# Kernel tuning notes

Hardware: AMD Instinct MI355X
Metric: run time of the kernel (lower is better)

Reference implementation:

```python
import jax, jax.numpy as jnp
import numpy as np

G = 9.80665  # scipy.constants.g


def _xavier(key, fan_in, fan_out):
    std = np.sqrt(2.0 / (fan_in + fan_out))
    return jax.random.normal(key, (fan_in, fan_out), dtype=jnp.float32) * std


def setup_inputs() -> dict:
    key = jax.random.key(0)
    ks = jax.random.split(key, 16)
    n_samples, n_nodes, n_pipes, n_demand, hidden = 16384, 512, 1024, 256, 64
    D = jax.random.uniform(ks[0], (n_samples, n_demand), dtype=jnp.float32) * 0.01
    leak_id = jax.random.randint(ks[1], (n_samples, 1), 0, n_pipes)
    A0 = jax.random.normal(ks[2], (n_nodes, n_pipes), dtype=jnp.float32) * 0.1
    inv = jax.random.normal(ks[3], (n_nodes, n_pipes), dtype=jnp.float32) * 0.1
    M = jax.random.normal(ks[4], (n_nodes, n_pipes), dtype=jnp.float32) * 0.1
    supply = jax.random.uniform(ks[5], (n_pipes,), dtype=jnp.float32) * 10.0
    L = jax.random.uniform(ks[6], (n_pipes,), dtype=jnp.float32) * 900.0 + 100.0  # pipe length [m]
    d = jax.random.uniform(ks[7], (n_pipes,), dtype=jnp.float32) * 0.4 + 0.1      # diameter [m]
    C = jax.random.uniform(ks[8], (n_pipes,), dtype=jnp.float32) * 50.0 + 100.0   # HW coefficient
    demand_idx = jnp.arange(n_demand) * 2  # distinct node indices < n_nodes
    a = jnp.float32(0.01)   # leak area
    Cd = jnp.float32(0.75)  # discharge coefficient
    W1 = _xavier(ks[9], 1, hidden); b1 = jnp.zeros((hidden,), jnp.float32)
    W2 = _xavier(ks[10], hidden, hidden); b2 = jnp.zeros((hidden,), jnp.float32)
    W3 = _xavier(ks[11], hidden, 1); b3 = jnp.zeros((1,), jnp.float32)
    base = jax.random.normal(ks[12], (n_pipes,), dtype=jnp.float32) * 0.1
    return {"D": D, "leak_id": leak_id, "A0": A0, "inv": inv, "M": M,
            "supply": supply, "L": L, "d": d, "C": C, "a": a, "Cd": Cd,
            "W1": W1, "b1": b1, "W2": W2, "b2": b2, "W3": W3, "b3": b3,
            "base": base, "demand_idx": demand_idx}


def reference(D, leak_id, A0, inv, M, supply, L, d, C, a, Cd,
              W1, b1, W2, b2, W3, b3, base, demand_idx):
    S = D.shape[0]
    n_nodes, n_pipes = M.shape
    idx = leak_id[:, 0]  # [S] int, pipe index per sample

    # Net(leak_id): tanh MLP + lookup of per-pipe base value
    x = leak_id.astype(jnp.float32)                      # [S,1]
    h = jnp.tanh(x @ W1 + b1)
    h = jnp.tanh(h @ W2 + b2)
    net_out = base[idx][:, None] + (h @ W3 + b3)          # [S,1]

    # scatter-built demand / leakage / areas
    demand = jnp.zeros((S, n_nodes), jnp.float32).at[:, demand_idx].set(D)
    rows = jnp.arange(S)
    leakage = jnp.zeros((S, n_pipes), jnp.float32).at[rows, idx].set(net_out[:, 0])
    areas = jnp.zeros((S, n_pipes), jnp.float32).at[rows, idx].set(a)

    # q = inv.T @ (M @ leakage + demand)
    y = jnp.einsum('np,sp->sn', M, leakage) + demand      # [S,Nn]
    q = jnp.einsum('np,sn->sp', inv, y)                   # [S,Np]

    # Hazen-Williams head loss
    hL = jnp.sign(q) * 10.667 * C[None] ** (-1.852) * d[None] ** (-4.871) * L[None] * jnp.abs(q) ** 1.852
    H = jnp.einsum('np,sp->sn', inv, supply[None] - hL)   # [S,Nn]

    # leak demand d_leak = Cd * (M @ areas) * sqrt(2 g relu(H))  (safe sqrt)
    Hp = jax.nn.relu(H)
    sq = jnp.sqrt(jnp.where(Hp > 0, Hp, 1.0)) * (Hp > 0).astype(jnp.float32)
    d_leak = Cd * jnp.einsum('np,sp->sn', M, areas) * jnp.sqrt(jnp.float32(2.0 * G)) * sq

    residual = jnp.einsum('np,sp->sn', A0, q) - demand - d_leak
    return jnp.mean(residual ** 2)
```

## Files before the change

kernel.cpp:

```cpp
#include <hip/hip_runtime.h>
#include <math.h>

typedef _Float16 f16;
typedef _Float16 f16x4 __attribute__((ext_vector_type(4)));
typedef _Float16 f16x8 __attribute__((ext_vector_type(8)));
typedef float f32x4 __attribute__((ext_vector_type(4)));

#define S_TOTAL 16384
#define N_NODES 512
#define N_PIPES 1024
#define N_DEM   256
#define HIDDEN  64
#define T_SCALE 256.0f

#define GLOAD16(gsrc, ldst) \
    __builtin_amdgcn_global_load_lds((const __attribute__((address_space(1))) void*)(gsrc), \
                                     (__attribute__((address_space(3))) void*)(ldst), 16, 0, 0)
#define SBAR()  __builtin_amdgcn_s_barrier()
#define FENCE() asm volatile("" ::: "memory")
#define WAIT4() asm volatile("s_waitcnt vmcnt(4)" ::: "memory")
#define WAIT0() asm volatile("s_waitcnt vmcnt(0)" ::: "memory")

__global__ __launch_bounds__(256) void prep_all(
    const float* __restrict__ W1, const float* __restrict__ b1,
    const float* __restrict__ W2, const float* __restrict__ b2,
    const float* __restrict__ W3, const float* __restrict__ b3,
    const float* __restrict__ base,
    const float* __restrict__ L, const float* __restrict__ dpipe,
    const float* __restrict__ Cw,
    const float* __restrict__ Mf, const float* __restrict__ inv,
    const float* __restrict__ A0, const float* __restrict__ D,
    const int* __restrict__ dmap,
    float* __restrict__ net, float* __restrict__ lKc,
    f16* __restrict__ MT16, f16* __restrict__ invT16,
    f16* __restrict__ inv16, f16* __restrict__ A016, f16* __restrict__ D16,
    f16* __restrict__ DI16, f16* __restrict__ IDXT,
    float* __restrict__ out, int out_size)
{
    __shared__ __align__(16) f16 tile[64][72];
    const int b = blockIdx.x, t = threadIdx.x;
    if (b < 256) {
        if (b == 0) for (int i = t; i < out_size; i += 256) out[i] = 0.f;
        const int wid = t >> 6, k = t & 63;
        const int p = b * 4 + wid;
        const float x = (float)p;
        float h1 = tanhf(x * W1[k] + b1[k]);
        float acc = b2[k];
        #pragma unroll
        for (int j = 0; j < HIDDEN; ++j) {
            float hj = __shfl(h1, j, 64);
            acc = fmaf(hj, W2[j * HIDDEN + k], acc);
        }
        float partial = tanhf(acc) * W3[k];
        #pragma unroll
        for (int off = 32; off > 0; off >>= 1) partial += __shfl_down(partial, off, 64);
        if (k == 0) {
            net[p] = base[p] + partial + b3[0];
            lKc[p] = log2f(10.667f) - 1.852f * log2f(Cw[p]) - 4.871f * log2f(dpipe[p]) + log2f(L[p]);
        }
        return;
    }
    if (b < 512) {
        const int idx = b - 256;
        const float* in = (idx < 128) ? Mf : inv;
        f16* outp = (idx < 128) ? MT16 : invT16;
        const int i2 = idx & 127;
        const int bx = i2 & 15, by = i2 >> 4;
        const int r0 = by * 64, c0 = bx * 64;
        const int lr = t / 16, lc4 = (t % 16) * 4;
        #pragma unroll
        for (int i = 0; i < 4; ++i) {
            int r = lr + i * 16;
            float4 v = *(const float4*)(in + (size_t)(r0 + r) * N_PIPES + c0 + lc4);
            tile[lc4 + 0][r] = (f16)v.x; tile[lc4 + 1][r] = (f16)v.y;
            tile[lc4 + 2][r] = (f16)v.z; tile[lc4 + 3][r] = (f16)v.w;
        }
        __syncthreads();
        const int wrow = t / 4, wc16 = (t % 4) * 16;
        *(f16x8*)(outp + (size_t)(c0 + wrow) * N_NODES + r0 + wc16)     = *(f16x8*)&tile[wrow][wc16];
        *(f16x8*)(outp + (size_t)(c0 + wrow) * N_NODES + r0 + wc16 + 8) = *(f16x8*)&tile[wrow][wc16 + 8];
        return;
    }
    const int tid = (b - 512) * 256 + t;
    const int np = 768 * 256;
    for (int i = tid; i < (N_NODES * N_PIPES) / 4; i += np) {
        float4 v = ((const float4*)inv)[i];
        ((f16x4*)inv16)[i] = (f16x4){(f16)v.x, (f16)v.y, (f16)v.z, (f16)v.w};
        float4 w = ((const float4*)A0)[i];
        ((f16x4*)A016)[i] = (f16x4){(f16)w.x, (f16)w.y, (f16)w.z, (f16)w.w};
    }
    for (int i = tid; i < (S_TOTAL * N_DEM) / 4; i += np) {
        float4 v = ((const float4*)D)[i];
        ((f16x4*)D16)[i] = (f16x4){(f16)v.x, (f16)v.y, (f16)v.z, (f16)v.w};
    }
    for (int i = tid; i < N_DEM * (N_PIPES / 4); i += np) {
        int j = i >> 8, p0 = (i & 255) * 4;
        float4 v = *(const float4*)(inv + (size_t)dmap[j] * N_PIPES + p0);
        *(f16x4*)(DI16 + (size_t)j * N_PIPES + p0) = (f16x4){(f16)v.x, (f16)v.y, (f16)v.z, (f16)v.w};
    }
    for (int i = tid; i < N_PIPES * (N_DEM / 4); i += np) {
        int p = i >> 6, j0 = (i & 63) * 4;
        f16x4 o;
        #pragma unroll
        for (int u = 0; u < 4; ++u)
            o[u] = (f16)inv[(size_t)dmap[j0 + u] * N_PIPES + p];
        *(f16x4*)(IDXT + (size_t)p * N_DEM + j0) = o;
    }
}

struct GemmP {
    const f16* A; int lda;
    const f16* B; int ldb;
    f16* C; int ldc;
    int K;
    const int* dmap;
    int gx, gy;
};

__device__ __forceinline__ void gemm_body(const GemmP& P, int bx, int by) {
    __shared__ __align__(16) f16 As[128][72], Bs[64][72];
    const int m0 = by * 128, c0 = bx * 64;
    const int t = threadIdx.x, lane = t & 63, wid = t >> 6;
    const int wr = wid >> 1, wc = wid & 1;
    const int cl = lane & 15, g = lane >> 4;
    const int tr = t >> 3, tc = (t & 7) * 8;
    f32x4 acc[4][2] = {};
    for (int k0 = 0; k0 < P.K; k0 += 64) {
        #pragma unroll
        for (int r = 0; r < 4; ++r) {
            int row = r * 32 + tr;
            *(f16x8*)&As[row][tc] = *(const f16x8*)(P.A + (size_t)(m0 + row) * P.lda + k0 + tc);
        }
        #pragma unroll
        for (int r = 0; r < 2; ++r) {
            int row = r * 32 + tr;
            *(f16x8*)&Bs[row][tc] = *(const f16x8*)(P.B + (size_t)(c0 + row) * P.ldb + k0 + tc);
        }
        __syncthreads();
        #pragma unroll
        for (int kk = 0; kk < 2; ++kk) {
            const int kb = kk * 32 + g * 8;
            f16x8 a[4], bfr[2];
            #pragma unroll
            for (int m = 0; m < 4; ++m) a[m] = *(const f16x8*)&As[wr * 64 + m * 16 + cl][kb];
            #pragma unroll
            for (int n = 0; n < 2; ++n) bfr[n] = *(const f16x8*)&Bs[wc * 32 + n * 16 + cl][kb];
            #pragma unroll
            for (int m = 0; m < 4; ++m)
                #pragma unroll
                for (int n = 0; n < 2; ++n)
                    acc[m][n] = __builtin_amdgcn_mfma_f32_16x16x32_f16(a[m], bfr[n], acc[m][n], 0, 0, 0);
        }
        __syncthreads();
    }
    #pragma unroll
    for (int m = 0; m < 4; ++m)
        #pragma unroll
        for (int reg = 0; reg < 4; ++reg) {
            const int row = m0 + wr * 64 + m * 16 + g * 4 + reg;
            #pragma unroll
            for (int n = 0; n < 2; ++n) {
                const int col = c0 + wc * 32 + n * 16 + cl;
                float v = acc[m][n][reg];
                if (P.dmap && P.dmap[col] == row) v -= 1.0f;
                P.C[(size_t)row * P.ldc + col] = (f16)v;
            }
        }
}

__global__ __launch_bounds__(256) void gemm_small3(GemmP p0, GemmP p1, GemmP p2) {
    const GemmP& P = (blockIdx.z == 0) ? p0 : (blockIdx.z == 1) ? p1 : p2;
    if ((int)blockIdx.x >= P.gx || (int)blockIdx.y >= P.gy) return;
    gemm_body(P, blockIdx.x, blockIdx.y);
}

__global__ __launch_bounds__(256) void gemm_small1(GemmP p0) {
    gemm_body(p0, blockIdx.x, blockIdx.y);
}

__global__ __launch_bounds__(512, 4) void gemm_qt_mfma(
    const f16* __restrict__ D16, const int* __restrict__ leak_id,
    const f16* __restrict__ IDXT, const float* __restrict__ net,
    const f16* __restrict__ G16, const float* __restrict__ lKc,
    const float* __restrict__ supply, f16* __restrict__ t16)
{
    __shared__ __align__(16) f16 As[2][128][64];
    __shared__ __align__(16) f16 Bs[2][128][64];
    const int nwg = gridDim.x * gridDim.y;
    const int bid = blockIdx.y * gridDim.x + blockIdx.x;
    const int w = (bid & 7) * (nwg >> 3) + (bid >> 3);
    const int bx = w % gridDim.x, by = w / gridDim.x;
    const int p0 = bx * 128, sb = by * 128;
    const int t = threadIdx.x, lane = t & 63, wid = t >> 6;
    const int wr = wid >> 2, wc = wid & 3;
    const int cl = lane & 15, g = lane >> 4;
    const int swrow = lane >> 3;
    const int swcol = ((lane & 7) ^ swrow) * 8;
    const int sx0 = ((g) ^ (cl & 7)) * 8;
    const int sx1 = ((4 + g) ^ (cl & 7)) * 8;

    const f16* Abase = D16 + (size_t)(sb + swrow) * N_DEM + swcol;
    const f16* Bbase = IDXT + (size_t)(p0 + swrow) * N_DEM + swcol;

    f32x4 acc[4][2] = {};
    auto stage = [&](int buf, int k0) {
        #pragma unroll
        for (int c = 0; c < 2; ++c) {
            int r0 = c * 64 + wid * 8;
            GLOAD16(Abase + (size_t)r0 * N_DEM + k0, &As[buf][r0][0]);
        }
        #pragma unroll
        for (int c = 0; c < 2; ++c) {
            int r0 = c * 64 + wid * 8;
            GLOAD16(Bbase + (size_t)r0 * N_DEM + k0, &Bs[buf][r0][0]);
        }
    };
    auto compute = [&](int buf) {
        #pragma unroll
        for (int kk = 0; kk < 2; ++kk) {
            const int sx = kk ? sx1 : sx0;
            f16x8 a[4], b[2];
            #pragma unroll
            for (int m = 0; m < 4; ++m) a[m] = *(const f16x8*)&As[buf][wr * 64 + m * 16 + cl][sx];
            #pragma unroll
            for (int n = 0; n < 2; ++n) b[n] = *(const f16x8*)&Bs[buf][wc * 32 + n * 16 + cl][sx];
            #pragma unroll
            for (int m = 0; m < 4; ++m)
                #pragma unroll
                for (int n = 0; n < 2; ++n)
                    acc[m][n] = __builtin_amdgcn_mfma_f32_16x16x32_f16(a[m], b[n], acc[m][n], 0, 0, 0);
        }
    };

    int cur = 0;
    stage(0, 0);
    #pragma unroll 1
    for (int k = 0; k < 3; ++k) {
        stage(cur ^ 1, (k + 1) * 64);
        WAIT4(); SBAR();
        compute(cur);
        FENCE(); SBAR();
        cur ^= 1;
    }
    WAIT0(); SBAR();
    compute(cur);

    float lKc2[2], sup2[2]; int pcol[2];
    #pragma unroll
    for (int n = 0; n < 2; ++n) {
        pcol[n] = p0 + wc * 32 + n * 16 + cl;
        lKc2[n] = lKc[pcol[n]]; sup2[n] = supply[pcol[n]];
    }
    #pragma unroll
    for (int m = 0; m < 4; ++m) {
        #pragma unroll
        for (int reg = 0; reg < 4; ++reg) {
            const int srow = sb + wr * 64 + m * 16 + g * 4 + reg;
            const int idx = leak_id[srow];
            const float nv = net[idx];
            #pragma unroll
            for (int n = 0; n < 2; ++n) {
                float qv = acc[m][n][reg] + nv * (float)G16[(size_t)idx * N_PIPES + pcol[n]];
                float l = __builtin_amdgcn_logf(fabsf(qv));
                float hL = copysignf(__builtin_amdgcn_exp2f(fmaf(1.852f, l, lKc2[n])), qv);
                t16[(size_t)srow * N_PIPES + pcol[n]] = (f16)((sup2[n] - hL) * (1.0f / T_SCALE));
            }
        }
    }
}

__global__ __launch_bounds__(512, 4) void gemm_res_mfma(
    const f16* __restrict__ t16, const f16* __restrict__ inv16,
    const f16* __restrict__ D16, const f16* __restrict__ P1p,
    const f16* __restrict__ MT16, const f16* __restrict__ G2_16,
    const int* __restrict__ leak_id, const float* __restrict__ net,
    const float* __restrict__ Cd_p, const float* __restrict__ a_p,
    float scale, float* __restrict__ out)
{
    __shared__ __align__(16) f16 As[2][128][64];
    __shared__ __align__(16) f16 Bs[2][128][64];
    const int nwg = gridDim.x * gridDim.y;
    const int bid = blockIdx.y * gridDim.x + blockIdx.x;
    const int w = (bid & 7) * (nwg >> 3) + (bid >> 3);
    const int bx = w % gridDim.x, by = w / gridDim.x;
    const int n0 = bx * 128, sb = by * 128;
    const int t = threadIdx.x, lane = t & 63, wid = t >> 6;
    const int wr = wid >> 2, wc = wid & 3;
    const int cl = lane & 15, g = lane >> 4;
    const int swrow = lane >> 3;
    const int swcol = ((lane & 7) ^ swrow) * 8;
    const int sx0 = ((g) ^ (cl & 7)) * 8;
    const int sx1 = ((4 + g) ^ (cl & 7)) * 8;

    const f16* HAb = t16   + (size_t)(sb + swrow) * N_PIPES + swcol;
    const f16* HBb = inv16 + (size_t)(n0 + swrow) * N_PIPES + swcol;
    const f16* RAb = D16   + (size_t)(sb + swrow) * N_DEM + swcol;
    const f16* RBb = P1p   + (size_t)(n0 + swrow) * N_DEM + swcol;

    f32x4 accH[4][2] = {}, accR[4][2] = {};

    auto stageH = [&](int buf, int k0) {
        #pragma unroll
        for (int c = 0; c < 2; ++c) {
            int r0 = c * 64 + wid * 8;
            GLOAD16(HAb + (size_t)r0 * N_PIPES + k0, &As[buf][r0][0]);
        }
        #pragma unroll
        for (int c = 0; c < 2; ++c) {
            int r0 = c * 64 + wid * 8;
            GLOAD16(HBb + (size_t)r0 * N_PIPES + k0, &Bs[buf][r0][0]);
        }
    };
    auto stageR = [&](int buf, int k0) {
        #pragma unroll
        for (int c = 0; c < 2; ++c) {
            int r0 = c * 64 + wid * 8;
            GLOAD16(RAb + (size_t)r0 * N_DEM + k0, &As[buf][r0][0]);
        }
        #pragma unroll
        for (int c = 0; c < 2; ++c) {
            int r0 = c * 64 + wid * 8;
            GLOAD16(RBb + (size_t)r0 * N_DEM + k0, &Bs[buf][r0][0]);
        }
    };
    auto computeT = [&](int buf, f32x4 (&accA)[4][2]) {
        #pragma unroll
        for (int kk = 0; kk < 2; ++kk) {
            const int sx = kk ? sx1 : sx0;
            f16x8 a[4], b[2];
            #pragma unroll
            for (int m = 0; m < 4; ++m) a[m] = *(const f16x8*)&As[buf][wr * 64 + m * 16 + cl][sx];
            #pragma unroll
            for (int n = 0; n < 2; ++n) b[n] = *(const f16x8*)&Bs[buf][wc * 32 + n * 16 + cl][sx];
            #pragma unroll
            for (int m = 0; m < 4; ++m)
                #pragma unroll
                for (int n = 0; n < 2; ++n)
                    accA[m][n] = __builtin_amdgcn_mfma_f32_16x16x32_f16(a[m], b[n], accA[m][n], 0, 0, 0);
        }
    };

    int cur = 0;
    stageH(0, 0);
    #pragma unroll 1
    for (int k = 0; k < 15; ++k) {
        stageH(cur ^ 1, (k + 1) * 64);
        WAIT4(); SBAR();
        computeT(cur, accH);
        FENCE(); SBAR();
        cur ^= 1;
    }
    stageR(cur ^ 1, 0);
    WAIT4(); SBAR();
    computeT(cur, accH);
    FENCE(); SBAR();
    cur ^= 1;
    #pragma unroll 1
    for (int k = 0; k < 3; ++k) {
        stageR(cur ^ 1, (k + 1) * 64);
        WAIT4(); SBAR();
        computeT(cur, accR);
        FENCE(); SBAR();
        cur ^= 1;
    }
    WAIT0(); SBAR();
    computeT(cur, accR);

    const float cda = Cd_p[0] * a_p[0] * sqrtf(2.f * 9.80665f);
    int node[2];
    #pragma unroll
    for (int n = 0; n < 2; ++n) node[n] = n0 + wc * 32 + n * 16 + cl;
    float lsum = 0.f;
    #pragma unroll
    for (int m = 0; m < 4; ++m) {
        #pragma unroll
        for (int reg = 0; reg < 4; ++reg) {
            const int srow = sb + wr * 64 + m * 16 + g * 4 + reg;
            const int idx = leak_id[srow];
            const float nv = net[idx];
            #pragma unroll
            for (int n = 0; n < 2; ++n) {
                const float H = accH[m][n][reg] * T_SCALE;
                const float sq = (H > 0.f) ? sqrtf(H) : 0.f;
                const float dl = cda * (float)MT16[(size_t)idx * N_NODES + node[n]] * sq;
                const float r = accR[m][n][reg] + nv * (float)G2_16[(size_t)idx * N_NODES + node[n]] - dl;
                lsum += r * r;
            }
        }
    }
    #pragma unroll
    for (int off = 32; off > 0; off >>= 1) lsum += __shfl_down(lsum, off, 64);
    __syncthreads();
    float* wred = (float*)&As[0][0][0];
    if (lane == 0) wred[wid] = lsum;
    __syncthreads();
    if (t == 0) {
        float tot = 0.f;
        #pragma unroll
        for (int i = 0; i < 8; ++i) tot += wred[i];
        atomicAdd(out, tot * scale);
    }
}

extern "C" void kernel_launch(void* const* d_in, const int* in_sizes, int n_in,
                              void* d_out, int out_size, void* d_ws, size_t ws_size,
                              hipStream_t stream) {
    const float* D          = (const float*)d_in[0];
    const int*   leak_id    = (const int*)  d_in[1];
    const float* A0         = (const float*)d_in[2];
    const float* inv        = (const float*)d_in[3];
    const float* M          = (const float*)d_in[4];
    const float* supply     = (const float*)d_in[5];
    const float* L          = (const float*)d_in[6];
    const float* dpipe      = (const float*)d_in[7];
    const float* C          = (const float*)d_in[8];
    const float* a_p        = (const float*)d_in[9];
    const float* Cd_p       = (const float*)d_in[10];
    const float* W1         = (const float*)d_in[11];
    const float* b1         = (const float*)d_in[12];
    const float* W2         = (const float*)d_in[13];
    const float* b2         = (const float*)d_in[14];
    const float* W3         = (const float*)d_in[15];
    const float* b3         = (const float*)d_in[16];
    const float* base       = (const float*)d_in[17];
    const int*   demand_idx = (const int*)  d_in[18];

    char* ws = (char*)d_ws;
    size_t off = 0;
    auto carve = [&](size_t bytes) { char* p = ws + off; off += (bytes + 255) & ~(size_t)255; return p; };
    float* net    = (float*)carve(N_PIPES * 4);
    float* lKc    = (float*)carve(N_PIPES * 4);
    f16* inv16  = (f16*)carve((size_t)N_NODES * N_PIPES * 2);
    f16* A016   = (f16*)carve((size_t)N_NODES * N_PIPES * 2);
    f16* MT16   = (f16*)carve((size_t)N_PIPES * N_NODES * 2);
    f16* invT16 = (f16*)carve((size_t)N_PIPES * N_NODES * 2);
    f16* G16    = (f16*)carve((size_t)N_PIPES * N_PIPES * 2);
    f16* G2_16  = (f16*)carve((size_t)N_PIPES * N_NODES * 2);
    f16* Wt     = (f16*)carve((size_t)N_NODES * N_NODES * 2);
    f16* P1p    = (f16*)carve((size_t)N_NODES * N_DEM * 2);
    f16* DI16   = (f16*)carve((size_t)N_DEM * N_PIPES * 2);
    f16* IDXT   = (f16*)carve((size_t)N_PIPES * N_DEM * 2);
    f16* D16    = (f16*)carve((size_t)S_TOTAL * N_DEM * 2);
    f16* t16    = (f16*)carve((size_t)S_TOTAL * N_PIPES * 2);

    prep_all<<<1280, 256, 0, stream>>>(
        W1, b1, W2, b2, W3, b3, base, L, dpipe, C,
        M, inv, A0, D, demand_idx,
        net, lKc, MT16, invT16, inv16, A016, D16, DI16, IDXT,
        (float*)d_out, out_size);

    GemmP pG16 = {MT16, N_NODES, invT16, N_NODES, G16, N_PIPES, N_NODES, nullptr, 16, 8};
    GemmP pWt  = {A016, N_PIPES, inv16, N_PIPES, Wt, N_NODES, N_PIPES, nullptr, 8, 4};
    GemmP pP1  = {A016, N_PIPES, DI16, N_PIPES, P1p, N_DEM, N_PIPES, demand_idx, 4, 4};
    gemm_small3<<<dim3(16, 8, 3), 256, 0, stream>>>(pG16, pWt, pP1);

    GemmP pG2 = {MT16, N_NODES, Wt, N_NODES, G2_16, N_NODES, N_NODES, nullptr, 8, 8};
    gemm_small1<<<dim3(8, 8), 256, 0, stream>>>(pG2);

    gemm_qt_mfma<<<dim3(N_PIPES / 128, S_TOTAL / 128), 512, 0, stream>>>(
        D16, leak_id, IDXT, net, G16, lKc, supply, t16);
    const float scale = 1.f / ((float)S_TOTAL * (float)N_NODES);
    gemm_res_mfma<<<dim3(N_NODES / 128, S_TOTAL / 128), 512, 0, stream>>>(
        t16, inv16, D16, P1p, MT16, G2_16, leak_id, net, Cd_p, a_p,
        scale, (float*)d_out);
}
```

Measured before the change: 97.16 us.

## Convert D to fp16 inside GEMM tiles and fold G2 GEMM into qt launch

The separate fp16 conversion of D in the prep kernel is removed. The q-GEMM and the residual GEMM now load fp32 D rows from global memory, convert them in registers and write them into a single swizzled LDS tile, using a new wait/barrier pipeline. The small MT·Wt GEMM (G2) is no longer its own launch; it runs as extra blocks appended to the q-GEMM grid (blockIdx.y >= 128). This saves one launch, the D16 write/read round trip and some prep work, but it reads twice as many bytes for D and adds register-staged loads with manual vmcnt accounting, which risks ordering mistakes.

```diff
diff --git a/kernel.cpp b/kernel.cpp
--- a/kernel.cpp
+++ b/kernel.cpp
@@ -18,8 +18,8 @@
                                      (__attribute__((address_space(3))) void*)(ldst), 16, 0, 0)
 #define SBAR()  __builtin_amdgcn_s_barrier()
 #define FENCE() asm volatile("" ::: "memory")
-#define WAIT4() asm volatile("s_waitcnt vmcnt(4)" ::: "memory")
-#define WAIT0() asm volatile("s_waitcnt vmcnt(0)" ::: "memory")
+#define WAITN(n) asm volatile("s_waitcnt vmcnt(" #n ")" ::: "memory")
+#define LGKM0() asm volatile("s_waitcnt lgkmcnt(0)" ::: "memory")
 
 __global__ __launch_bounds__(256) void prep_all(
     const float* __restrict__ W1, const float* __restrict__ b1,
@@ -29,11 +29,11 @@
     const float* __restrict__ L, const float* __restrict__ dpipe,
     const float* __restrict__ Cw,
     const float* __restrict__ Mf, const float* __restrict__ inv,
-    const float* __restrict__ A0, const float* __restrict__ D,
+    const float* __restrict__ A0,
     const int* __restrict__ dmap,
     float* __restrict__ net, float* __restrict__ lKc,
     f16* __restrict__ MT16, f16* __restrict__ invT16,
-    f16* __restrict__ inv16, f16* __restrict__ A016, f16* __restrict__ D16,
+    f16* __restrict__ inv16, f16* __restrict__ A016,
     f16* __restrict__ DI16, f16* __restrict__ IDXT,
     float* __restrict__ out, int out_size)
 {
@@ -82,16 +82,12 @@
         return;
     }
     const int tid = (b - 512) * 256 + t;
-    const int np = 768 * 256;
+    const int np = 512 * 256;
     for (int i = tid; i < (N_NODES * N_PIPES) / 4; i += np) {
         float4 v = ((const float4*)inv)[i];
         ((f16x4*)inv16)[i] = (f16x4){(f16)v.x, (f16)v.y, (f16)v.z, (f16)v.w};
         float4 w = ((const float4*)A0)[i];
         ((f16x4*)A016)[i] = (f16x4){(f16)w.x, (f16)w.y, (f16)w.z, (f16)w.w};
-    }
-    for (int i = tid; i < (S_TOTAL * N_DEM) / 4; i += np) {
-        float4 v = ((const float4*)D)[i];
-        ((f16x4*)D16)[i] = (f16x4){(f16)v.x, (f16)v.y, (f16)v.z, (f16)v.w};
     }
     for (int i = tid; i < N_DEM * (N_PIPES / 4); i += np) {
         int j = i >> 8, p0 = (i & 255) * 4;
@@ -174,56 +170,103 @@
     gemm_body(P, blockIdx.x, blockIdx.y);
 }
 
-__global__ __launch_bounds__(256) void gemm_small1(GemmP p0) {
-    gemm_body(p0, blockIdx.x, blockIdx.y);
-}
-
 __global__ __launch_bounds__(512, 4) void gemm_qt_mfma(
-    const f16* __restrict__ D16, const int* __restrict__ leak_id,
+    const float* __restrict__ Df, const int* __restrict__ leak_id,
     const f16* __restrict__ IDXT, const float* __restrict__ net,
     const f16* __restrict__ G16, const float* __restrict__ lKc,
-    const float* __restrict__ supply, f16* __restrict__ t16)
+    const float* __restrict__ supply, f16* __restrict__ t16,
+    const f16* __restrict__ MT16, const f16* __restrict__ Wt,
+    f16* __restrict__ G2out)
 {
-    __shared__ __align__(16) f16 As[2][128][64];
-    __shared__ __align__(16) f16 Bs[2][128][64];
-    const int nwg = gridDim.x * gridDim.y;
-    const int bid = blockIdx.y * gridDim.x + blockIdx.x;
-    const int w = (bid & 7) * (nwg >> 3) + (bid >> 3);
-    const int bx = w % gridDim.x, by = w / gridDim.x;
+    __shared__ __align__(16) f16 AsM[128 * 64];
+    __shared__ __align__(16) f16 BsM[2][128 * 64];
+    const int t = threadIdx.x, lane = t & 63, wid = t >> 6;
+
+    if (blockIdx.y >= 128) {
+        f16 (*A2)[72] = (f16(*)[72])&BsM[0][0];
+        f16 (*B2)[72] = (f16(*)[72])&AsM[0];
+        const int m0 = ((int)blockIdx.y - 128) * 128, c0 = blockIdx.x * 64;
+        const int wr = wid >> 2, wc = wid & 3;
+        const int cl = lane & 15, g = lane >> 4;
+        f32x4 acc[4] = {};
+        for (int k0 = 0; k0 < 512; k0 += 64) {
+            {
+                int r = t >> 2, c16 = (t & 3) * 16;
+                *(f16x8*)&A2[r][c16]     = *(const f16x8*)(MT16 + (size_t)(m0 + r) * N_NODES + k0 + c16);
+                *(f16x8*)&A2[r][c16 + 8] = *(const f16x8*)(MT16 + (size_t)(m0 + r) * N_NODES + k0 + c16 + 8);
+                int r2 = t >> 3, c8 = (t & 7) * 8;
+                *(f16x8*)&B2[r2][c8] = *(const f16x8*)(Wt + (size_t)(c0 + r2) * N_NODES + k0 + c8);
+            }
+            __syncthreads();
+            #pragma unroll
+            for (int kk = 0; kk < 2; ++kk) {
+                const int kb = kk * 32 + g * 8;
+                f16x8 b = *(const f16x8*)&B2[wc * 16 + cl][kb];
+                #pragma unroll
+                for (int m = 0; m < 4; ++m) {
+                    f16x8 a = *(const f16x8*)&A2[wr * 64 + m * 16 + cl][kb];
+                    acc[m] = __builtin_amdgcn_mfma_f32_16x16x32_f16(a, b, acc[m], 0, 0, 0);
+                }
+            }
+            __syncthreads();
+        }
+        #pragma unroll
+        for (int m = 0; m < 4; ++m)
+            #pragma unroll
+            for (int reg = 0; reg < 4; ++reg)
+                G2out[(size_t)(m0 + wr * 64 + m * 16 + g * 4 + reg) * N_NODES + c0 + wc * 16 + cl] = (f16)acc[m][reg];
+        return;
+    }
+    const int bid = blockIdx.y * 8 + blockIdx.x;
+    const int w = (bid & 7) * 128 + (bid >> 3);
+    const int bx = w & 7, by = w >> 3;
     const int p0 = bx * 128, sb = by * 128;
-    const int t = threadIdx.x, lane = t & 63, wid = t >> 6;
     const int wr = wid >> 2, wc = wid & 3;
     const int cl = lane & 15, g = lane >> 4;
     const int swrow = lane >> 3;
-    const int swcol = ((lane & 7) ^ swrow) * 8;
-    const int sx0 = ((g) ^ (cl & 7)) * 8;
-    const int sx1 = ((4 + g) ^ (cl & 7)) * 8;
-
-    const f16* Abase = D16 + (size_t)(sb + swrow) * N_DEM + swcol;
-    const f16* Bbase = IDXT + (size_t)(p0 + swrow) * N_DEM + swcol;
-
-    f32x4 acc[4][2] = {};
-    auto stage = [&](int buf, int k0) {
+    const int swp = ((lane & 7) ^ swrow) * 8;
+    const int sx0 = (g ^ (cl & 7)) * 8, sx1 = ((4 + g) ^ (cl & 7)) * 8;
+
+    f16 (*As)[64] = (f16(*)[64])AsM;
+    const f16* Bbase = IDXT + (size_t)(p0 + swrow) * N_DEM + swp;
+
+    const int arow = t >> 2, ah = t & 3;
+    const int s0 = 2 * ah, s1 = 2 * ah + 1;
+    const int gc0 = (s0 ^ (arow & 7)) * 8, gc1 = (s1 ^ (arow & 7)) * 8;
+    const float* Drow = Df + (size_t)(sb + arow) * N_DEM;
+
+    float4 a01, a02, a11, a12;
+    auto A_load = [&](int k0) {
+        a01 = *(const float4*)(Drow + k0 + gc0);
+        a02 = *(const float4*)(Drow + k0 + gc0 + 4);
+        a11 = *(const float4*)(Drow + k0 + gc1);
+        a12 = *(const float4*)(Drow + k0 + gc1 + 4);
+    };
+    auto A_write = [&]() {
+        f16x8 v0 = {(f16)a01.x, (f16)a01.y, (f16)a01.z, (f16)a01.w,
+                    (f16)a02.x, (f16)a02.y, (f16)a02.z, (f16)a02.w};
+        f16x8 v1 = {(f16)a11.x, (f16)a11.y, (f16)a11.z, (f16)a11.w,
+                    (f16)a12.x, (f16)a12.y, (f16)a12.z, (f16)a12.w};
+        *(f16x8*)&As[arow][s0 * 8] = v0;
+        *(f16x8*)&As[arow][s1 * 8] = v1;
+    };
+    auto B_stage = [&](int buf, int k0) {
         #pragma unroll
         for (int c = 0; c < 2; ++c) {
             int r0 = c * 64 + wid * 8;
-            GLOAD16(Abase + (size_t)r0 * N_DEM + k0, &As[buf][r0][0]);
-        }
-        #pragma unroll
-        for (int c = 0; c < 2; ++c) {
-            int r0 = c * 64 + wid * 8;
-            GLOAD16(Bbase + (size_t)r0 * N_DEM + k0, &Bs[buf][r0][0]);
-        }
-    };
+            GLOAD16(Bbase + (size_t)r0 * N_DEM + k0, &BsM[buf][r0 * 64]);
+        }
+    };
+    f32x4 acc[4][2] = {};
     auto compute = [&](int buf) {
         #pragma unroll
         for (int kk = 0; kk < 2; ++kk) {
             const int sx = kk ? sx1 : sx0;
             f16x8 a[4], b[2];
             #pragma unroll
-            for (int m = 0; m < 4; ++m) a[m] = *(const f16x8*)&As[buf][wr * 64 + m * 16 + cl][sx];
-            #pragma unroll
-            for (int n = 0; n < 2; ++n) b[n] = *(const f16x8*)&Bs[buf][wc * 32 + n * 16 + cl][sx];
+            for (int m = 0; m < 4; ++m) a[m] = *(const f16x8*)&As[wr * 64 + m * 16 + cl][sx];
+            #pragma unroll
+            for (int n = 0; n < 2; ++n) b[n] = *(const f16x8*)&BsM[buf][(wc * 32 + n * 16 + cl) * 64 + sx];
             #pragma unroll
             for (int m = 0; m < 4; ++m)
                 #pragma unroll
@@ -232,18 +275,19 @@
         }
     };
 
+    A_load(0); B_stage(0, 0);
     int cur = 0;
-    stage(0, 0);
     #pragma unroll 1
-    for (int k = 0; k < 3; ++k) {
-        stage(cur ^ 1, (k + 1) * 64);
-        WAIT4(); SBAR();
+    for (int k = 0; k < 4; ++k) {
+        WAITN(2);
+        SBAR();
+        A_write(); LGKM0();
+        if (k < 3) { A_load((k + 1) * 64); B_stage(cur ^ 1, (k + 1) * 64); WAITN(6); }
+        else       { WAITN(0); }
+        SBAR();
         compute(cur);
-        FENCE(); SBAR();
         cur ^= 1;
     }
-    WAIT0(); SBAR();
-    compute(cur);
 
     float lKc2[2], sup2[2]; int pcol[2];
     #pragma unroll
@@ -271,14 +315,14 @@
 
 __global__ __launch_bounds__(512, 4) void gemm_res_mfma(
     const f16* __restrict__ t16, const f16* __restrict__ inv16,
-    const f16* __restrict__ D16, const f16* __restrict__ P1p,
+    const float* __restrict__ Df, const f16* __restrict__ P1p,
     const f16* __restrict__ MT16, const f16* __restrict__ G2_16,
     const int* __restrict__ leak_id, const float* __restrict__ net,
     const float* __restrict__ Cd_p, const float* __restrict__ a_p,
     float scale, float* __restrict__ out)
 {
-    __shared__ __align__(16) f16 As[2][128][64];
-    __shared__ __align__(16) f16 Bs[2][128][64];
+    __shared__ __align__(16) f16 AsM[2][128 * 64];
+    __shared__ __align__(16) f16 BsM[2][128 * 64];
     const int nwg = gridDim.x * gridDim.y;
     const int bid = blockIdx.y * gridDim.x + blockIdx.x;
     const int w = (bid & 7) * (nwg >> 3) + (bid >> 3);
@@ -288,14 +332,12 @@
     const int wr = wid >> 2, wc = wid & 3;
     const int cl = lane & 15, g = lane >> 4;
     const int swrow = lane >> 3;
-    const int swcol = ((lane & 7) ^ swrow) * 8;
-    const int sx0 = ((g) ^ (cl & 7)) * 8;
-    const int sx1 = ((4 + g) ^ (cl & 7)) * 8;
-
-    const f16* HAb = t16   + (size_t)(sb + swrow) * N_PIPES + swcol;
-    const f16* HBb = inv16 + (size_t)(n0 + swrow) * N_PIPES + swcol;
-    const f16* RAb = D16   + (size_t)(sb + swrow) * N_DEM + swcol;
-    const f16* RBb = P1p   + (size_t)(n0 + swrow) * N_DEM + swcol;
+    const int swp = ((lane & 7) ^ swrow) * 8;
+    const int sx0 = (g ^ (cl & 7)) * 8, sx1 = ((4 + g) ^ (cl & 7)) * 8;
+
+    const f16* HAb = t16   + (size_t)(sb + swrow) * N_PIPES + swp;
+    const f16* HBb = inv16 + (size_t)(n0 + swrow) * N_PIPES + swp;
+    const f16* RBb = P1p   + (size_t)(n0 + swrow) * N_DEM + swp;
 
     f32x4 accH[4][2] = {}, accR[4][2] = {};
 
@@ -303,40 +345,28 @@
         #pragma unroll
         for (int c = 0; c < 2; ++c) {
             int r0 = c * 64 + wid * 8;
-            GLOAD16(HAb + (size_t)r0 * N_PIPES + k0, &As[buf][r0][0]);
+            GLOAD16(HAb + (size_t)r0 * N_PIPES + k0, &AsM[buf][r0 * 64]);
         }
         #pragma unroll
         for (int c = 0; c < 2; ++c) {
             int r0 = c * 64 + wid * 8;
-            GLOAD16(HBb + (size_t)r0 * N_PIPES + k0, &Bs[buf][r0][0]);
-        }
-    };
-    auto stageR = [&](int buf, int k0) {
-        #pragma unroll
-        for (int c = 0; c < 2; ++c) {
-            int r0 = c * 64 + wid * 8;
-            GLOAD16(RAb + (size_t)r0 * N_DEM + k0, &As[buf][r0][0]);
-        }
-        #pragma unroll
-        for (int c = 0; c < 2; ++c) {
-            int r0 = c * 64 + wid * 8;
-            GLOAD16(RBb + (size_t)r0 * N_DEM + k0, &Bs[buf][r0][0]);
-        }
-    };
-    auto computeT = [&](int buf, f32x4 (&accA)[4][2]) {
+            GLOAD16(HBb + (size_t)r0 * N_PIPES + k0, &BsM[buf][r0 * 64]);
+        }
+    };
+    auto computeH = [&](int buf) {
         #pragma unroll
         for (int kk = 0; kk < 2; ++kk) {
             const int sx = kk ? sx1 : sx0;
             f16x8 a[4], b[2];
             #pragma unroll
-            for (int m = 0; m < 4; ++m) a[m] = *(const f16x8*)&As[buf][wr * 64 + m * 16 + cl][sx];
-            #pragma unroll
-            for (int n = 0; n < 2; ++n) b[n] = *(const f16x8*)&Bs[buf][wc * 32 + n * 16 + cl][sx];
+            for (int m = 0; m < 4; ++m) a[m] = *(const f16x8*)&AsM[buf][(wr * 64 + m * 16 + cl) * 64 + sx];
+            #pragma unroll
+            for (int n = 0; n < 2; ++n) b[n] = *(const f16x8*)&BsM[buf][(wc * 32 + n * 16 + cl) * 64 + sx];
             #pragma unroll
             for (int m = 0; m < 4; ++m)
                 #pragma unroll
                 for (int n = 0; n < 2; ++n)
-                    accA[m][n] = __builtin_amdgcn_mfma_f32_16x16x32_f16(a[m], b[n], accA[m][n], 0, 0, 0);
+                    accH[m][n] = __builtin_amdgcn_mfma_f32_16x16x32_f16(a[m], b[n], accH[m][n], 0, 0, 0);
         }
     };
 
@@ -345,26 +375,73 @@
     #pragma unroll 1
     for (int k = 0; k < 15; ++k) {
         stageH(cur ^ 1, (k + 1) * 64);
-        WAIT4(); SBAR();
-        computeT(cur, accH);
+        WAITN(4); SBAR();
+        computeH(cur);
         FENCE(); SBAR();
         cur ^= 1;
     }
-    stageR(cur ^ 1, 0);
-    WAIT4(); SBAR();
-    computeT(cur, accH);
+    WAITN(0); SBAR();
+    computeH(cur);
     FENCE(); SBAR();
-    cur ^= 1;
+
+    const int arow = t >> 2, ah = t & 3;
+    const int s0 = 2 * ah, s1 = 2 * ah + 1;
+    const int gc0 = (s0 ^ (arow & 7)) * 8, gc1 = (s1 ^ (arow & 7)) * 8;
+    const float* Drow = Df + (size_t)(sb + arow) * N_DEM;
+    f16 (*Asr)[64] = (f16(*)[64])&AsM[0][0];
+
+    float4 a01, a02, a11, a12;
+    auto A_load = [&](int k0) {
+        a01 = *(const float4*)(Drow + k0 + gc0);
+        a02 = *(const float4*)(Drow + k0 + gc0 + 4);
+        a11 = *(const float4*)(Drow + k0 + gc1);
+        a12 = *(const float4*)(Drow + k0 + gc1 + 4);
+    };
+    auto A_write = [&]() {
+        f16x8 v0 = {(f16)a01.x, (f16)a01.y, (f16)a01.z, (f16)a01.w,
+                    (f16)a02.x, (f16)a02.y, (f16)a02.z, (f16)a02.w};
+        f16x8 v1 = {(f16)a11.x, (f16)a11.y, (f16)a11.z, (f16)a11.w,
+                    (f16)a12.x, (f16)a12.y, (f16)a12.z, (f16)a12.w};
+        *(f16x8*)&Asr[arow][s0 * 8] = v0;
+        *(f16x8*)&Asr[arow][s1 * 8] = v1;
+    };
+    auto B_stageR = [&](int buf, int k0) {
+        #pragma unroll
+        for (int c = 0; c < 2; ++c) {
+            int r0 = c * 64 + wid * 8;
+            GLOAD16(RBb + (size_t)r0 * N_DEM + k0, &BsM[buf][r0 * 64]);
+        }
+    };
+    auto computeR = [&](int buf) {
+        #pragma unroll
+        for (int kk = 0; kk < 2; ++kk) {
+            const int sx = kk ? sx1 : sx0;
+            f16x8 a[4], b[2];
+            #pragma unroll
+            for (int m = 0; m < 4; ++m) a[m] = *(const f16x8*)&Asr[wr * 64 + m * 16 + cl][sx];
+            #pragma unroll
+            for (int n = 0; n < 2; ++n) b[n] = *(const f16x8*)&BsM[buf][(wc * 32 + n * 16 + cl) * 64 + sx];
+            #pragma unroll
+            for (int m = 0; m < 4; ++m)
+                #pragma unroll
+                for (int n = 0; n < 2; ++n)
+                    accR[m][n] = __builtin_amdgcn_mfma_f32_16x16x32_f16(a[m], b[n], accR[m][n], 0, 0, 0);
+        }
+    };
+
+    A_load(0); B_stageR(0, 0);
+    int cur2 = 0;
     #pragma unroll 1
-    for (int k = 0; k < 3; ++k) {
-        stageR(cur ^ 1, (k + 1) * 64);
-        WAIT4(); SBAR();
-        computeT(cur, accR);
-        FENCE(); SBAR();
-        cur ^= 1;
-    }
-    WAIT0(); SBAR();
-    computeT(cur, accR);
+    for (int k = 0; k < 4; ++k) {
+        WAITN(2);
+        SBAR();
+        A_write(); LGKM0();
+        if (k < 3) { A_load((k + 1) * 64); B_stageR(cur2 ^ 1, (k + 1) * 64); WAITN(6); }
+        else       { WAITN(0); }
+        SBAR();
+        computeR(cur2);
+        cur2 ^= 1;
+    }
 
     const float cda = Cd_p[0] * a_p[0] * sqrtf(2.f * 9.80665f);
     int node[2];
@@ -391,7 +468,7 @@
     #pragma unroll
     for (int off = 32; off > 0; off >>= 1) lsum += __shfl_down(lsum, off, 64);
     __syncthreads();
-    float* wred = (float*)&As[0][0][0];
+    float* wred = (float*)&AsM[0][0];
     if (lane == 0) wred[wid] = lsum;
     __syncthreads();
     if (t == 0) {
@@ -440,13 +517,12 @@
     f16* P1p    = (f16*)carve((size_t)N_NODES * N_DEM * 2);
     f16* DI16   = (f16*)carve((size_t)N_DEM * N_PIPES * 2);
     f16* IDXT   = (f16*)carve((size_t)N_PIPES * N_DEM * 2);
-    f16* D16    = (f16*)carve((size_t)S_TOTAL * N_DEM * 2);
     f16* t16    = (f16*)carve((size_t)S_TOTAL * N_PIPES * 2);
 
-    prep_all<<<1280, 256, 0, stream>>>(
+    prep_all<<<1024, 256, 0, stream>>>(
         W1, b1, W2, b2, W3, b3, base, L, dpipe, C,
-        M, inv, A0, D, demand_idx,
-        net, lKc, MT16, invT16, inv16, A016, D16, DI16, IDXT,
+        M, inv, A0, demand_idx,
+        net, lKc, MT16, invT16, inv16, A016, DI16, IDXT,
         (float*)d_out, out_size);
 
     GemmP pG16 = {MT16, N_NODES, invT16, N_NODES, G16, N_PIPES, N_NODES, nullptr, 16, 8};
@@ -454,13 +530,11 @@
     GemmP pP1  = {A016, N_PIPES, DI16, N_PIPES, P1p, N_DEM, N_PIPES, demand_idx, 4, 4};
     gemm_small3<<<dim3(16, 8, 3), 256, 0, stream>>>(pG16, pWt, pP1);
 
-    GemmP pG2 = {MT16, N_NODES, Wt, N_NODES, G2_16, N_NODES, N_NODES, nullptr, 8, 8};
-    gemm_small1<<<dim3(8, 8), 256, 0, stream>>>(pG2);
-
-    gemm_qt_mfma<<<dim3(N_PIPES / 128, S_TOTAL / 128), 512, 0, stream>>>(
-        D16, leak_id, IDXT, net, G16, lKc, supply, t16);
+    gemm_qt_mfma<<<dim3(8, 136), 512, 0, stream>>>(
+        D, leak_id, IDXT, net, G16, lKc, supply, t16, MT16, Wt, G2_16);
+
     const float scale = 1.f / ((float)S_TOTAL * (float)N_NODES);
     gemm_res_mfma<<<dim3(N_NODES / 128, S_TOTAL / 128), 512, 0, stream>>>(
-        t16, inv16, D16, P1p, MT16, G2_16, leak_id, net, Cd_p, a_p,
+        t16, inv16, D, P1p, MT16, G2_16, leak_id, net, Cd_p, a_p,
         scale, (float*)d_out);
 }
```

New measurement: 98.60 us. About the same (+1.5%).

## Fuse q/head-loss GEMM with residual GEMM, keeping t tile in LDS

Applied to the files above, without the earlier changes.

Merges the two large GEMM kernels into one kernel where each block owns 64 samples. It computes q and the Hazen-Williams transform per 64-pipe chunk into a double-buffered LDS tile, then accumulates H over all 512 nodes directly. This removes the 32 MB t16 intermediate write and read and one launch. The cost is a grid of only 256 blocks with occupancy 2, and B operands (IDXT, inv16, P1p) read straight from global without LDS staging, which may hurt latency hiding and MFMA utilisation.

```diff
diff --git a/kernel.cpp b/kernel.cpp
--- a/kernel.cpp
+++ b/kernel.cpp
@@ -13,13 +13,7 @@
 #define HIDDEN  64
 #define T_SCALE 256.0f
 
-#define GLOAD16(gsrc, ldst) \
-    __builtin_amdgcn_global_load_lds((const __attribute__((address_space(1))) void*)(gsrc), \
-                                     (__attribute__((address_space(3))) void*)(ldst), 16, 0, 0)
-#define SBAR()  __builtin_amdgcn_s_barrier()
-#define FENCE() asm volatile("" ::: "memory")
-#define WAIT4() asm volatile("s_waitcnt vmcnt(4)" ::: "memory")
-#define WAIT0() asm volatile("s_waitcnt vmcnt(0)" ::: "memory")
+#define MFMA16(a, b, c) __builtin_amdgcn_mfma_f32_16x16x32_f16(a, b, c, 0, 0, 0)
 
 __global__ __launch_bounds__(256) void prep_all(
     const float* __restrict__ W1, const float* __restrict__ b1,
@@ -149,7 +143,7 @@
             for (int m = 0; m < 4; ++m)
                 #pragma unroll
                 for (int n = 0; n < 2; ++n)
-                    acc[m][n] = __builtin_amdgcn_mfma_f32_16x16x32_f16(a[m], bfr[n], acc[m][n], 0, 0, 0);
+                    acc[m][n] = MFMA16(a[m], bfr[n], acc[m][n]);
         }
         __syncthreads();
     }
@@ -178,212 +172,121 @@
     gemm_body(p0, blockIdx.x, blockIdx.y);
 }
 
-__global__ __launch_bounds__(512, 4) void gemm_qt_mfma(
+__global__ __launch_bounds__(512, 2) void qtres_fused(
     const f16* __restrict__ D16, const int* __restrict__ leak_id,
     const f16* __restrict__ IDXT, const float* __restrict__ net,
     const f16* __restrict__ G16, const float* __restrict__ lKc,
-    const float* __restrict__ supply, f16* __restrict__ t16)
-{
-    __shared__ __align__(16) f16 As[2][128][64];
-    __shared__ __align__(16) f16 Bs[2][128][64];
-    const int nwg = gridDim.x * gridDim.y;
-    const int bid = blockIdx.y * gridDim.x + blockIdx.x;
-    const int w = (bid & 7) * (nwg >> 3) + (bid >> 3);
-    const int bx = w % gridDim.x, by = w / gridDim.x;
-    const int p0 = bx * 128, sb = by * 128;
-    const int t = threadIdx.x, lane = t & 63, wid = t >> 6;
-    const int wr = wid >> 2, wc = wid & 3;
-    const int cl = lane & 15, g = lane >> 4;
-    const int swrow = lane >> 3;
-    const int swcol = ((lane & 7) ^ swrow) * 8;
-    const int sx0 = ((g) ^ (cl & 7)) * 8;
-    const int sx1 = ((4 + g) ^ (cl & 7)) * 8;
-
-    const f16* Abase = D16 + (size_t)(sb + swrow) * N_DEM + swcol;
-    const f16* Bbase = IDXT + (size_t)(p0 + swrow) * N_DEM + swcol;
-
-    f32x4 acc[4][2] = {};
-    auto stage = [&](int buf, int k0) {
-        #pragma unroll
-        for (int c = 0; c < 2; ++c) {
-            int r0 = c * 64 + wid * 8;
-            GLOAD16(Abase + (size_t)r0 * N_DEM + k0, &As[buf][r0][0]);
-        }
-        #pragma unroll
-        for (int c = 0; c < 2; ++c) {
-            int r0 = c * 64 + wid * 8;
-            GLOAD16(Bbase + (size_t)r0 * N_DEM + k0, &Bs[buf][r0][0]);
-        }
-    };
-    auto compute = [&](int buf) {
-        #pragma unroll
-        for (int kk = 0; kk < 2; ++kk) {
-            const int sx = kk ? sx1 : sx0;
-            f16x8 a[4], b[2];
-            #pragma unroll
-            for (int m = 0; m < 4; ++m) a[m] = *(const f16x8*)&As[buf][wr * 64 + m * 16 + cl][sx];
-            #pragma unroll
-            for (int n = 0; n < 2; ++n) b[n] = *(const f16x8*)&Bs[buf][wc * 32 + n * 16 + cl][sx];
-            #pragma unroll
-            for (int m = 0; m < 4; ++m)
-                #pragma unroll
-                for (int n = 0; n < 2; ++n)
-                    acc[m][n] = __builtin_amdgcn_mfma_f32_16x16x32_f16(a[m], b[n], acc[m][n], 0, 0, 0);
-        }
-    };
-
-    int cur = 0;
-    stage(0, 0);
-    #pragma unroll 1
-    for (int k = 0; k < 3; ++k) {
-        stage(cur ^ 1, (k + 1) * 64);
-        WAIT4(); SBAR();
-        compute(cur);
-        FENCE(); SBAR();
-        cur ^= 1;
-    }
-    WAIT0(); SBAR();
-    compute(cur);
-
-    float lKc2[2], sup2[2]; int pcol[2];
-    #pragma unroll
-    for (int n = 0; n < 2; ++n) {
-        pcol[n] = p0 + wc * 32 + n * 16 + cl;
-        lKc2[n] = lKc[pcol[n]]; sup2[n] = supply[pcol[n]];
-    }
-    #pragma unroll
-    for (int m = 0; m < 4; ++m) {
-        #pragma unroll
-        for (int reg = 0; reg < 4; ++reg) {
-            const int srow = sb + wr * 64 + m * 16 + g * 4 + reg;
-            const int idx = leak_id[srow];
-            const float nv = net[idx];
-            #pragma unroll
-            for (int n = 0; n < 2; ++n) {
-                float qv = acc[m][n][reg] + nv * (float)G16[(size_t)idx * N_PIPES + pcol[n]];
-                float l = __builtin_amdgcn_logf(fabsf(qv));
-                float hL = copysignf(__builtin_amdgcn_exp2f(fmaf(1.852f, l, lKc2[n])), qv);
-                t16[(size_t)srow * N_PIPES + pcol[n]] = (f16)((sup2[n] - hL) * (1.0f / T_SCALE));
-            }
-        }
-    }
-}
-
-__global__ __launch_bounds__(512, 4) void gemm_res_mfma(
-    const f16* __restrict__ t16, const f16* __restrict__ inv16,
-    const f16* __restrict__ D16, const f16* __restrict__ P1p,
+    const float* __restrict__ supply,
+    const f16* __restrict__ inv16, const f16* __restrict__ P1p,
     const f16* __restrict__ MT16, const f16* __restrict__ G2_16,
-    const int* __restrict__ leak_id, const float* __restrict__ net,
     const float* __restrict__ Cd_p, const float* __restrict__ a_p,
     float scale, float* __restrict__ out)
 {
-    __shared__ __align__(16) f16 As[2][128][64];
-    __shared__ __align__(16) f16 Bs[2][128][64];
-    const int nwg = gridDim.x * gridDim.y;
-    const int bid = blockIdx.y * gridDim.x + blockIdx.x;
-    const int w = (bid & 7) * (nwg >> 3) + (bid >> 3);
-    const int bx = w % gridDim.x, by = w / gridDim.x;
-    const int n0 = bx * 128, sb = by * 128;
-    const int t = threadIdx.x, lane = t & 63, wid = t >> 6;
-    const int wr = wid >> 2, wc = wid & 3;
+    __shared__ __align__(16) f16 Ds[64][264];
+    __shared__ __align__(16) f16 tq[2][64][72];
+    const int sb = blockIdx.x * 64;
+    const int t = threadIdx.x, lane = t & 63, w = t >> 6;
     const int cl = lane & 15, g = lane >> 4;
-    const int swrow = lane >> 3;
-    const int swcol = ((lane & 7) ^ swrow) * 8;
-    const int sx0 = ((g) ^ (cl & 7)) * 8;
-    const int sx1 = ((4 + g) ^ (cl & 7)) * 8;
-
-    const f16* HAb = t16   + (size_t)(sb + swrow) * N_PIPES + swcol;
-    const f16* HBb = inv16 + (size_t)(n0 + swrow) * N_PIPES + swcol;
-    const f16* RAb = D16   + (size_t)(sb + swrow) * N_DEM + swcol;
-    const f16* RBb = P1p   + (size_t)(n0 + swrow) * N_DEM + swcol;
-
-    f32x4 accH[4][2] = {}, accR[4][2] = {};
-
-    auto stageH = [&](int buf, int k0) {
-        #pragma unroll
-        for (int c = 0; c < 2; ++c) {
-            int r0 = c * 64 + wid * 8;
-            GLOAD16(HAb + (size_t)r0 * N_PIPES + k0, &As[buf][r0][0]);
-        }
-        #pragma unroll
-        for (int c = 0; c < 2; ++c) {
-            int r0 = c * 64 + wid * 8;
-            GLOAD16(HBb + (size_t)r0 * N_PIPES + k0, &Bs[buf][r0][0]);
-        }
-    };
-    auto stageR = [&](int buf, int k0) {
-        #pragma unroll
-        for (int c = 0; c < 2; ++c) {
-            int r0 = c * 64 + wid * 8;
-            GLOAD16(RAb + (size_t)r0 * N_DEM + k0, &As[buf][r0][0]);
-        }
-        #pragma unroll
-        for (int c = 0; c < 2; ++c) {
-            int r0 = c * 64 + wid * 8;
-            GLOAD16(RBb + (size_t)r0 * N_DEM + k0, &Bs[buf][r0][0]);
-        }
-    };
-    auto computeT = [&](int buf, f32x4 (&accA)[4][2]) {
-        #pragma unroll
-        for (int kk = 0; kk < 2; ++kk) {
-            const int sx = kk ? sx1 : sx0;
-            f16x8 a[4], b[2];
-            #pragma unroll
-            for (int m = 0; m < 4; ++m) a[m] = *(const f16x8*)&As[buf][wr * 64 + m * 16 + cl][sx];
-            #pragma unroll
-            for (int n = 0; n < 2; ++n) b[n] = *(const f16x8*)&Bs[buf][wc * 32 + n * 16 + cl][sx];
-            #pragma unroll
-            for (int m = 0; m < 4; ++m)
+    const int wq_r = w >> 2, wq_c = w & 3;
+
+    {
+        const int row = t >> 3, c0 = (t & 7) * 32;
+        const f16* src = D16 + (size_t)(sb + row) * N_DEM + c0;
+        #pragma unroll
+        for (int u = 0; u < 4; ++u)
+            *(f16x8*)&Ds[row][c0 + u * 8] = *(const f16x8*)(src + u * 8);
+    }
+    int idxQ[2][4]; float nvQ[2][4];
+    #pragma unroll
+    for (int m = 0; m < 2; ++m)
+        #pragma unroll
+        for (int reg = 0; reg < 4; ++reg) {
+            idxQ[m][reg] = leak_id[sb + 32 * wq_r + m * 16 + g * 4 + reg];
+            nvQ[m][reg] = net[idxQ[m][reg]];
+        }
+    __syncthreads();
+
+    f32x4 accH[4][4] = {}, accR[4][4] = {};
+
+    #pragma unroll 1
+    for (int pc = 0; pc < 16; ++pc) {
+        const int p0 = pc * 64;
+        const int bp = p0 + wq_c * 16 + cl;
+        f32x4 aq0 = {0.f, 0.f, 0.f, 0.f}, aq1 = {0.f, 0.f, 0.f, 0.f};
+        #pragma unroll
+        for (int ks = 0; ks < 8; ++ks) {
+            const int kb = ks * 32 + g * 8;
+            f16x8 bq = *(const f16x8*)(IDXT + (size_t)bp * N_DEM + kb);
+            f16x8 a0 = *(const f16x8*)&Ds[32 * wq_r + cl][kb];
+            f16x8 a1 = *(const f16x8*)&Ds[32 * wq_r + 16 + cl][kb];
+            aq0 = MFMA16(a0, bq, aq0);
+            aq1 = MFMA16(a1, bq, aq1);
+        }
+        {
+            const float lk = lKc[bp], sup = supply[bp];
+            #pragma unroll
+            for (int m = 0; m < 2; ++m) {
                 #pragma unroll
-                for (int n = 0; n < 2; ++n)
-                    accA[m][n] = __builtin_amdgcn_mfma_f32_16x16x32_f16(a[m], b[n], accA[m][n], 0, 0, 0);
-        }
-    };
-
-    int cur = 0;
-    stageH(0, 0);
-    #pragma unroll 1
-    for (int k = 0; k < 15; ++k) {
-        stageH(cur ^ 1, (k + 1) * 64);
-        WAIT4(); SBAR();
-        computeT(cur, accH);
-        FENCE(); SBAR();
-        cur ^= 1;
-    }
-    stageR(cur ^ 1, 0);
-    WAIT4(); SBAR();
-    computeT(cur, accH);
-    FENCE(); SBAR();
-    cur ^= 1;
-    #pragma unroll 1
-    for (int k = 0; k < 3; ++k) {
-        stageR(cur ^ 1, (k + 1) * 64);
-        WAIT4(); SBAR();
-        computeT(cur, accR);
-        FENCE(); SBAR();
-        cur ^= 1;
-    }
-    WAIT0(); SBAR();
-    computeT(cur, accR);
+                for (int reg = 0; reg < 4; ++reg) {
+                    const int srow = 32 * wq_r + m * 16 + g * 4 + reg;
+                    float qv = (m ? aq1[reg] : aq0[reg]) +
+                               nvQ[m][reg] * (float)G16[(size_t)idxQ[m][reg] * N_PIPES + bp];
+                    float l = __builtin_amdgcn_logf(fabsf(qv));
+                    float hL = copysignf(__builtin_amdgcn_exp2f(fmaf(1.852f, l, lk)), qv);
+                    tq[pc & 1][srow][wq_c * 16 + cl] = (f16)((sup - hL) * (1.0f / T_SCALE));
+                }
+            }
+        }
+        __syncthreads();
+        #pragma unroll
+        for (int ks = 0; ks < 2; ++ks) {
+            const int kb = ks * 32 + g * 8;
+            f16x8 bh[4];
+            #pragma unroll
+            for (int fn = 0; fn < 4; ++fn)
+                bh[fn] = *(const f16x8*)(inv16 + (size_t)(w * 64 + fn * 16 + cl) * N_PIPES + p0 + kb);
+            #pragma unroll
+            for (int m = 0; m < 4; ++m) {
+                f16x8 a = *(const f16x8*)&tq[pc & 1][m * 16 + cl][kb];
+                #pragma unroll
+                for (int fn = 0; fn < 4; ++fn)
+                    accH[m][fn] = MFMA16(a, bh[fn], accH[m][fn]);
+            }
+        }
+    }
+
+    #pragma unroll
+    for (int ks = 0; ks < 8; ++ks) {
+        const int kb = ks * 32 + g * 8;
+        f16x8 br[4];
+        #pragma unroll
+        for (int fn = 0; fn < 4; ++fn)
+            br[fn] = *(const f16x8*)(P1p + (size_t)(w * 64 + fn * 16 + cl) * N_DEM + kb);
+        #pragma unroll
+        for (int m = 0; m < 4; ++m) {
+            f16x8 a = *(const f16x8*)&Ds[m * 16 + cl][kb];
+            #pragma unroll
+            for (int fn = 0; fn < 4; ++fn)
+                accR[m][fn] = MFMA16(a, br[fn], accR[m][fn]);
+        }
+    }
 
     const float cda = Cd_p[0] * a_p[0] * sqrtf(2.f * 9.80665f);
-    int node[2];
-    #pragma unroll
-    for (int n = 0; n < 2; ++n) node[n] = n0 + wc * 32 + n * 16 + cl;
     float lsum = 0.f;
     #pragma unroll
     for (int m = 0; m < 4; ++m) {
         #pragma unroll
         for (int reg = 0; reg < 4; ++reg) {
-            const int srow = sb + wr * 64 + m * 16 + g * 4 + reg;
-            const int idx = leak_id[srow];
+            const int srow = m * 16 + g * 4 + reg;
+            const int idx = leak_id[sb + srow];
             const float nv = net[idx];
             #pragma unroll
-            for (int n = 0; n < 2; ++n) {
-                const float H = accH[m][n][reg] * T_SCALE;
+            for (int fn = 0; fn < 4; ++fn) {
+                const int node = w * 64 + fn * 16 + cl;
+                const float H = accH[m][fn][reg] * T_SCALE;
                 const float sq = (H > 0.f) ? sqrtf(H) : 0.f;
-                const float dl = cda * (float)MT16[(size_t)idx * N_NODES + node[n]] * sq;
-                const float r = accR[m][n][reg] + nv * (float)G2_16[(size_t)idx * N_NODES + node[n]] - dl;
+                const float dl = cda * (float)MT16[(size_t)idx * N_NODES + node] * sq;
+                const float r = accR[m][fn][reg] + nv * (float)G2_16[(size_t)idx * N_NODES + node] - dl;
                 lsum += r * r;
             }
         }
@@ -391,8 +294,8 @@
     #pragma unroll
     for (int off = 32; off > 0; off >>= 1) lsum += __shfl_down(lsum, off, 64);
     __syncthreads();
-    float* wred = (float*)&As[0][0][0];
-    if (lane == 0) wred[wid] = lsum;
+    float* wred = (float*)&Ds[0][0];
+    if (lane == 0) wred[w] = lsum;
     __syncthreads();
     if (t == 0) {
         float tot = 0.f;
@@ -441,7 +344,6 @@
     f16* DI16   = (f16*)carve((size_t)N_DEM * N_PIPES * 2);
     f16* IDXT   = (f16*)carve((size_t)N_PIPES * N_DEM * 2);
     f16* D16    = (f16*)carve((size_t)S_TOTAL * N_DEM * 2);
-    f16* t16    = (f16*)carve((size_t)S_TOTAL * N_PIPES * 2);
 
     prep_all<<<1280, 256, 0, stream>>>(
         W1, b1, W2, b2, W3, b3, base, L, dpipe, C,
@@ -457,10 +359,8 @@
     GemmP pG2 = {MT16, N_NODES, Wt, N_NODES, G2_16, N_NODES, N_NODES, nullptr, 8, 8};
     gemm_small1<<<dim3(8, 8), 256, 0, stream>>>(pG2);
 
-    gemm_qt_mfma<<<dim3(N_PIPES / 128, S_TOTAL / 128), 512, 0, stream>>>(
-        D16, leak_id, IDXT, net, G16, lKc, supply, t16);
     const float scale = 1.f / ((float)S_TOTAL * (float)N_NODES);
-    gemm_res_mfma<<<dim3(N_NODES / 128, S_TOTAL / 128), 512, 0, stream>>>(
-        t16, inv16, D16, P1p, MT16, G2_16, leak_id, net, Cd_p, a_p,
-        scale, (float*)d_out);
-}
+    qtres_fused<<<256, 512, 0, stream>>>(
+        D16, leak_id, IDXT, net, G16, lKc, supply,
+        inv16, P1p, MT16, G2_16, Cd_p, a_p, scale, (float*)d_out);
+}
```

New measurement: 162.7 us. +67.5%, slower.
